# Performance work log

Hardware: AMD Instinct MI355X
Metric: run time of the kernel (lower is better)

The kernel has to match this reference:

```python
import jax, jax.numpy as jnp
import numpy as np
from jax import lax

# sym8 analysis low-pass filter (pywt.Wavelet('sym8').dec_lo, matches MATLAB Lo_D)
FL = 16
DEC_LO = np.array([-0.0033824159510061256, -0.0005421323317911481, 0.03169508781149298,
                   0.007607487324917605, -0.1432942383508097, -0.061273359067658524,
                   0.4813596512583722, 0.7771857517005235, 0.3644418948353314,
                   -0.051945838107709037, -0.027219029917056003, 0.049137179673607506,
                   0.003808752013890615, -0.01495225833704823, -0.0003029205147213668,
                   0.0018899503327594609])
REC_LO = DEC_LO[::-1]
REC_HI = ((-1.0) ** np.arange(FL)) * DEC_LO  # qmf: rec_hi[k] = (-1)^k * rec_lo[FL-1-k]
DEC_HI = REC_HI[::-1]
# lax.conv does correlation, np.convolve flips -> store flipped filters
_DEC_K = jnp.asarray(np.stack([DEC_LO[::-1], DEC_HI[::-1]])[:, None, :], dtype=jnp.float32)  # (2,1,16)
_REC_K = jnp.asarray(np.stack([REC_LO[::-1], REC_HI[::-1]])[None, :, :], dtype=jnp.float32)  # (1,2,16)
DN = ('NCH', 'OIH', 'NCH')


def _dwt(x):
    # single-level pywt dwt, mode='symmetric': pad FL-1 each side, full conv, take odd indices
    B, C, S = x.shape
    xe = jnp.pad(x.reshape(B * C, 1, S), ((0, 0), (0, 0), (FL - 1, FL - 1)), mode='symmetric')[..., 1:]
    y = lax.conv_general_dilated(xe, _DEC_K, (2,), 'VALID', dimension_numbers=DN)
    L = y.shape[-1]  # floor((S + FL - 1)/2)
    y = y.reshape(B, C, 2, L)
    return y[:, :, 0], y[:, :, 1]


def _idwt(a, d):
    # single-level pywt idwt: upsample (len 2L-1), full conv, trim FL-2 each side
    B, C, L = a.shape
    c = jnp.stack([a, d], axis=2).reshape(B * C, 2, L)
    y = lax.conv_general_dilated(c, _REC_K, (1,), [(1, 1)], lhs_dilation=(2,), dimension_numbers=DN)
    return y.reshape(B, C, y.shape[-1])  # length 2L - FL + 2


def _wavedec(x, level):
    ds = []
    a = x
    for _ in range(level):
        a, d = _dwt(a)
        ds.append(d)
    return a, ds[::-1]  # coarsest first, matching pywt [cA_n, cD_n, ..., cD_1]


def _waverec(a, ds):
    for d in ds:
        if a.shape[-1] == d.shape[-1] + 1:  # static shapes -> Python if is jit-safe
            a = a[..., :-1]
        a = _idwt(a, d)
    return a


def _c1(x, w, b):
    # 1x1 conv: w (O,C), x (B,C,L)
    return jnp.einsum('oc,bcl->bol', w, x) + b[:, None]


def _inorm(x, eps=1e-5):
    m = jnp.mean(x, axis=-1, keepdims=True)
    v = jnp.mean((x - m) ** 2, axis=-1, keepdims=True)
    return (x - m) * lax.rsqrt(v + eps)


def _block(x, w_w, w_b, ca_w, ca_b, cd_w, cd_b, m1_w, m1_b, m2_w, m2_b):
    xn = _inorm(x)
    xs = lax.conv_general_dilated(xn, w_w, (1,), [(1, 1)], dimension_numbers=DN) + w_b[:, None]
    level = cd_w.shape[0]
    a, ds = _wavedec(xn, level)
    a = _c1(a, ca_w, ca_b)
    ds = [_c1(d, cd_w[i], cd_b[i]) for i, d in enumerate(ds)]
    xw = _waverec(a, ds)[..., : xs.shape[-1]]
    xo = x + jax.nn.gelu(xw + xs, approximate=False)
    xon = _inorm(xo)
    h = jax.nn.gelu(_c1(xon, m1_w, m1_b), approximate=False)
    return xo + _c1(h, m2_w, m2_b)


def _forward(x, lift_w, lift_b, blk_w_w, blk_w_b, blk_ca_w, blk_ca_b, blk_cd_w, blk_cd_b,
             blk_m1_w, blk_m1_b, blk_m2_w, blk_m2_b, p1_w, p1_b, p2_w, p2_b):
    B, S = x.shape
    grid = jnp.broadcast_to(jnp.linspace(-1.0, 1.0, S, dtype=x.dtype)[None, None, :], (B, 1, S))
    h = jnp.concatenate([x[:, None, :], grid], axis=1)  # (B, 2, S)
    h = _c1(h, lift_w, lift_b)
    for i in range(blk_w_w.shape[0]):
        h = _block(h, blk_w_w[i], blk_w_b[i], blk_ca_w[i], blk_ca_b[i], blk_cd_w[i],
                   blk_cd_b[i], blk_m1_w[i], blk_m1_b[i], blk_m2_w[i], blk_m2_b[i])
    h = jax.nn.gelu(_c1(h, p1_w, p1_b), approximate=False)
    return _c1(h, p2_w, p2_b)


def setup_inputs():
    key = jax.random.key(0)
    ks = jax.random.split(key, 17)
    B, S, C, NB, LV = 16, 8192, 64, 4, 4
    H = 2 * C  # mlp_expansion=2
    f = jnp.float32
    rn = lambda k, shape, s: jax.random.normal(k, shape, dtype=f) * s
    return {
        'x': jax.random.normal(ks[0], (B, S), dtype=f),
        'lift_w': rn(ks[1], (C, 2), 0.5), 'lift_b': rn(ks[2], (C,), 0.05),
        'blk_w_w': rn(ks[3], (NB, C, C, 3), 0.07), 'blk_w_b': rn(ks[4], (NB, C), 0.05),
        'blk_ca_w': rn(ks[5], (NB, C, C), 0.12), 'blk_ca_b': rn(ks[6], (NB, C), 0.05),
        'blk_cd_w': rn(ks[7], (NB, LV, C, C), 0.12), 'blk_cd_b': rn(ks[8], (NB, LV, C), 0.05),
        'blk_m1_w': rn(ks[9], (NB, H, C), 0.12), 'blk_m1_b': rn(ks[10], (NB, H), 0.05),
        'blk_m2_w': rn(ks[11], (NB, C, H), 0.08), 'blk_m2_b': rn(ks[12], (NB, C), 0.05),
        'p1_w': rn(ks[13], (C // 2, C), 0.12), 'p1_b': rn(ks[14], (C // 2,), 0.05),
        'p2_w': rn(ks[15], (C, C // 2), 0.17), 'p2_b': rn(ks[16], (C,), 0.05),
    }


def reference(x, lift_w, lift_b, blk_w_w, blk_w_b, blk_ca_w, blk_ca_b, blk_cd_w, blk_cd_b,
              blk_m1_w, blk_m1_b, blk_m2_w, blk_m2_b, p1_w, p1_b, p2_w, p2_b):
    return _forward(x, lift_w, lift_b, blk_w_w, blk_w_b, blk_ca_w, blk_ca_b, blk_cd_w,
                    blk_cd_b, blk_m1_w, blk_m1_b, blk_m2_w, blk_m2_b, p1_w, p1_b, p2_w, p2_b)
```

## Files before the change

### kernel.cpp

```cpp
#include <hip/hip_runtime.h>
#include <math.h>

#define S_LEN 8192
#define B_N   16
#define NBC   1024
#define L1v 4103
#define L2v 2059
#define L3v 1037
#define L4v 526
#define LP1 4104
#define LP2 2060
#define LP3 1040
#define LP4 528

typedef __attribute__((ext_vector_type(8))) short bf16x8;
typedef __attribute__((ext_vector_type(4))) float f32x4;

__constant__ float c_dlo[16] = {
    -0.0033824159510061256f, -0.0005421323317911481f,  0.03169508781149298f,
     0.007607487324917605f,  -0.1432942383508097f,    -0.061273359067658524f,
     0.4813596512583722f,     0.7771857517005235f,     0.3644418948353314f,
    -0.05194583810770904f,   -0.027219029917056003f,   0.049137179673607506f,
     0.003808752013890615f,  -0.01495225833704823f,   -0.0003029205147213668f,
     0.0018899503327594609f
};
__constant__ float c_dhi[16] = {
    -0.0018899503327594609f, -0.0003029205147213668f,  0.01495225833704823f,
     0.003808752013890615f,  -0.049137179673607506f,  -0.027219029917056003f,
     0.05194583810770904f,    0.3644418948353314f,    -0.7771857517005235f,
     0.4813596512583722f,     0.061273359067658524f,  -0.1432942383508097f,
    -0.007607487324917605f,   0.03169508781149298f,    0.0005421323317911481f,
    -0.0033824159510061256f
};

__device__ __forceinline__ float gelu1(float x) {
    return 0.5f * x * (1.0f + erff(x * 0.70710678118654752f));
}
__device__ __forceinline__ float4 load4g(const float* __restrict__ row, int l, int L) {
    float4 v;
    if (l >= 0 && l + 3 < L) {
        v = *(const float4*)(row + l);
    } else {
        v.x = (l     >= 0 && l     < L) ? row[l]     : 0.f;
        v.y = (l + 1 >= 0 && l + 1 < L) ? row[l + 1] : 0.f;
        v.z = (l + 2 >= 0 && l + 2 < L) ? row[l + 2] : 0.f;
        v.w = (l + 3 >= 0 && l + 3 < L) ? row[l + 3] : 0.f;
    }
    return v;
}
__device__ __forceinline__ void store4g(float* __restrict__ row, int l, int L, float4 v) {
    if (l + 3 < L) {
        *(float4*)(row + l) = v;
    } else {
        if (l     < L) row[l]     = v.x;
        if (l + 1 < L) row[l + 1] = v.y;
        if (l + 2 < L) row[l + 2] = v.z;
        if (l + 3 < L) row[l + 3] = v.w;
    }
}
__device__ __forceinline__ ushort f2bf(float f) {
    uint u = __float_as_uint(f);
    u += 0x7fffu + ((u >> 16) & 1u);
    return (ushort)(u >> 16);
}
__device__ __forceinline__ uint pack2bf(float a, float b) {
    return (uint)f2bf(a) | ((uint)f2bf(b) << 16);
}

__global__ __launch_bounds__(256) void lift_kernel(const float* __restrict__ x,
                                                   const float* __restrict__ w,
                                                   const float* __restrict__ bias,
                                                   float* __restrict__ out) {
    int idx = blockIdx.x * 256 + threadIdx.x;
    int s = idx & (S_LEN - 1);
    int r = idx >> 13;
    int o = r & 63;
    int b = r >> 6;
    float g = -1.0f + 2.0f * (float)s / (float)(S_LEN - 1);
    out[idx] = fmaf(w[o * 2 + 0], x[b * S_LEN + s], fmaf(w[o * 2 + 1], g, bias[o]));
}

__global__ __launch_bounds__(256) void stats_kernel(const float* __restrict__ in,
                                                    float2* __restrict__ stats) {
    const int base = blockIdx.x * S_LEN;
    const int tid = threadIdx.x;
    float s = 0.f, ss = 0.f;
#pragma unroll
    for (int i = 0; i < 8; ++i) {
        float4 v = *(const float4*)(in + base + (tid + i * 256) * 4);
        s += v.x + v.y + v.z + v.w;
        ss = fmaf(v.x, v.x, fmaf(v.y, v.y, fmaf(v.z, v.z, fmaf(v.w, v.w, ss))));
    }
    for (int off = 32; off > 0; off >>= 1) {
        s  += __shfl_down(s, off, 64);
        ss += __shfl_down(ss, off, 64);
    }
    __shared__ float sh[8];
    int lane = tid & 63, wv = tid >> 6;
    if (lane == 0) { sh[wv] = s; sh[4 + wv] = ss; }
    __syncthreads();
    if (tid == 0) {
        float tot  = sh[0] + sh[1] + sh[2] + sh[3];
        float tot2 = sh[4] + sh[5] + sh[6] + sh[7];
        float mean = tot * (1.0f / S_LEN);
        float var  = tot2 * (1.0f / S_LEN) - mean * mean;
        stats[blockIdx.x] = make_float2(mean, rsqrtf(var + 1e-5f));
    }
}

#define CWP 200
#define CXP 72

__global__ __launch_bounds__(256) void conv3_mfma_kernel(const float* __restrict__ in,
                                                         float* __restrict__ out,
                                                         const float* __restrict__ W,
                                                         const float* __restrict__ bias,
                                                         const float2* __restrict__ stats) {
    __shared__ ushort sW[64 * CWP];
    __shared__ ushort sXt[144 * CXP];
    const int b = blockIdx.y;
    const int n0 = blockIdx.x * 128;
    const int tid = threadIdx.x;

    {
        const int o = tid >> 2, q = tid & 3;
        const float* wsrc = W + o * 192;
        uint* dst = (uint*)(sW + o * CWP + q * 48);
#pragma unroll
        for (int i = 0; i < 12; ++i) {
            int k = q * 48 + i * 4;
            int tap = k >> 6, c = k & 63;
            float v0 = wsrc[c * 3 + tap];
            float v1 = wsrc[(c + 1) * 3 + tap];
            float v2 = wsrc[(c + 2) * 3 + tap];
            float v3 = wsrc[(c + 3) * 3 + tap];
            dst[2 * i]     = pack2bf(v0, v1);
            dst[2 * i + 1] = pack2bf(v2, v3);
        }
    }
    {
        const int ch = tid >> 2, q = tid & 3;
        const int rowi = b * 64 + ch;
        const float2 st = stats[rowi];
        const float* row = in + (size_t)rowi * S_LEN;
#pragma unroll
        for (int i = 0; i < 9; ++i) {
            int p = q * 36 + i * 4;
            int l = n0 - 8 + p;
            float4 v;
            if (l >= 0 && l + 3 < S_LEN) {
                v = *(const float4*)(row + l);
                v.x = (v.x - st.x) * st.y; v.y = (v.y - st.x) * st.y;
                v.z = (v.z - st.x) * st.y; v.w = (v.w - st.x) * st.y;
            } else {
                v.x = (l     >= 0 && l     < S_LEN) ? (row[l]     - st.x) * st.y : 0.f;
                v.y = (l + 1 >= 0 && l + 1 < S_LEN) ? (row[l + 1] - st.x) * st.y : 0.f;
                v.z = (l + 2 >= 0 && l + 2 < S_LEN) ? (row[l + 2] - st.x) * st.y : 0.f;
                v.w = (l + 3 >= 0 && l + 3 < S_LEN) ? (row[l + 3] - st.x) * st.y : 0.f;
            }
            sXt[(p + 0) * CXP + ch] = f2bf(v.x);
            sXt[(p + 1) * CXP + ch] = f2bf(v.y);
            sXt[(p + 2) * CXP + ch] = f2bf(v.z);
            sXt[(p + 3) * CXP + ch] = f2bf(v.w);
        }
    }
    __syncthreads();

    const int w = tid >> 6, l = tid & 63, g = l >> 4, c = l & 15;
    f32x4 acc[2][4];
#pragma unroll
    for (int mt = 0; mt < 4; ++mt) {
        float4 bv = *(const float4*)(bias + 16 * mt + 4 * g);
#pragma unroll
        for (int t = 0; t < 2; ++t) {
            acc[t][mt][0] = bv.x; acc[t][mt][1] = bv.y;
            acc[t][mt][2] = bv.z; acc[t][mt][3] = bv.w;
        }
    }
#pragma unroll
    for (int kk = 0; kk < 6; ++kk) {
        const int tap = kk >> 1;
        bf16x8 af[4];
#pragma unroll
        for (int mt = 0; mt < 4; ++mt)
            af[mt] = *(bf16x8*)(sW + (16 * mt + c) * CWP + kk * 32 + 8 * g);
#pragma unroll
        for (int t = 0; t < 2; ++t) {
            const int nl = 32 * w + 16 * t + c;
            const int p = nl + tap + 7;
            bf16x8 xb = *(bf16x8*)(sXt + p * CXP + (kk & 1) * 32 + 8 * g);
#pragma unroll
            for (int mt = 0; mt < 4; ++mt)
                acc[t][mt] = __builtin_amdgcn_mfma_f32_16x16x32_bf16(af[mt], xb, acc[t][mt], 0, 0, 0);
        }
    }
#pragma unroll
    for (int t = 0; t < 2; ++t) {
        const int nl = 32 * w + 16 * t + c;
#pragma unroll
        for (int mt = 0; mt < 4; ++mt)
#pragma unroll
            for (int r = 0; r < 4; ++r) {
                int m = 16 * mt + 4 * g + r;
                out[((size_t)(b * 64 + m)) * S_LEN + n0 + nl] = acc[t][mt][r];
            }
    }
}

#define WMP 72
#define WXP 136

__global__ __launch_bounds__(256) void wmix_kernel(float* __restrict__ d1,
                                                   float* __restrict__ d2,
                                                   float* __restrict__ d3,
                                                   float* __restrict__ d4,
                                                   float* __restrict__ a4,
                                                   const float* __restrict__ cd_w,
                                                   const float* __restrict__ cd_b,
                                                   const float* __restrict__ ca_w,
                                                   const float* __restrict__ ca_b) {
    __shared__ ushort sW[64 * WMP];
    __shared__ ushort sX[64 * WXP];
    const int b = blockIdx.y;
    const int t = blockIdx.x;
    float* buf; const float* W; const float* bias; int L, LP, l0;
    if (t < 33)      { buf = d1; W = cd_w + 3 * 4096; bias = cd_b + 3 * 64; L = L1v; LP = LP1; l0 = t * 128; }
    else if (t < 50) { buf = d2; W = cd_w + 2 * 4096; bias = cd_b + 2 * 64; L = L2v; LP = LP2; l0 = (t - 33) * 128; }
    else if (t < 59) { buf = d3; W = cd_w + 1 * 4096; bias = cd_b + 1 * 64; L = L3v; LP = LP3; l0 = (t - 50) * 128; }
    else if (t < 64) { buf = d4; W = cd_w;            bias = cd_b;          L = L4v; LP = LP4; l0 = (t - 59) * 128; }
    else             { buf = a4; W = ca_w;            bias = ca_b;          L = L4v; LP = LP4; l0 = (t - 64) * 128; }
    const int tid = threadIdx.x;
    {
        int row = tid >> 2, q = tid & 3;
        const float* src = W + row * 64 + q * 16;
        uint* dst = (uint*)(sW + row * WMP + q * 16);
#pragma unroll
        for (int i = 0; i < 4; ++i) {
            float4 v = *(const float4*)(src + 4 * i);
            dst[2 * i]     = pack2bf(v.x, v.y);
            dst[2 * i + 1] = pack2bf(v.z, v.w);
        }
    }
    {
        int ch = tid >> 2, part = tid & 3;
        const float* src = buf + ((size_t)(b * 64 + ch)) * LP;
        uint* dst = (uint*)(sX + ch * WXP + part * 32);
#pragma unroll
        for (int i = 0; i < 8; ++i) {
            int l = l0 + part * 32 + 4 * i;
            float4 v = load4g(src, l, L);
            dst[2 * i]     = pack2bf(v.x, v.y);
            dst[2 * i + 1] = pack2bf(v.z, v.w);
        }
    }
    __syncthreads();
    const int w = tid >> 6, l = tid & 63, g = l >> 4, c = l & 15;
    f32x4 acc[2][4];
#pragma unroll
    for (int mt = 0; mt < 4; ++mt) {
        float4 bv = *(const float4*)(bias + 16 * mt + 4 * g);
#pragma unroll
        for (int tt = 0; tt < 2; ++tt) {
            acc[tt][mt][0] = bv.x; acc[tt][mt][1] = bv.y;
            acc[tt][mt][2] = bv.z; acc[tt][mt][3] = bv.w;
        }
    }
#pragma unroll
    for (int kk = 0; kk < 2; ++kk) {
        bf16x8 af[4];
#pragma unroll
        for (int mt = 0; mt < 4; ++mt)
            af[mt] = *(bf16x8*)(sW + (16 * mt + c) * WMP + kk * 32 + 8 * g);
#pragma unroll
        for (int tt = 0; tt < 2; ++tt) {
            const int nl = 32 * w + 16 * tt + c;
            bf16x8 xb;
#pragma unroll
            for (int j = 0; j < 8; ++j)
                xb[j] = (short)sX[(kk * 32 + 8 * g + j) * WXP + nl];
#pragma unroll
            for (int mt = 0; mt < 4; ++mt)
                acc[tt][mt] = __builtin_amdgcn_mfma_f32_16x16x32_bf16(af[mt], xb, acc[tt][mt], 0, 0, 0);
        }
    }
#pragma unroll
    for (int tt = 0; tt < 2; ++tt) {
        const int nl = 32 * w + 16 * tt + c;
        if (l0 + nl < L) {
#pragma unroll
            for (int mt = 0; mt < 4; ++mt)
#pragma unroll
                for (int r = 0; r < 4; ++r) {
                    int m = 16 * mt + 4 * g + r;
                    buf[((size_t)(b * 64 + m)) * LP + l0 + nl] = acc[tt][mt][r];
                }
        }
    }
}

#define W1P 72
#define W2P 136
#define XP  66
#define MP  136

__global__ __launch_bounds__(256) void mlp_kernel(float* __restrict__ A,
                                                  const float2* __restrict__ stats,
                                                  const float* __restrict__ W1,
                                                  const float* __restrict__ b1,
                                                  const float* __restrict__ W2,
                                                  const float* __restrict__ b2) {
    __shared__ ushort sW1[128 * W1P];
    __shared__ ushort sW2[64 * W2P];
    __shared__ ushort sX [64 * XP];
    __shared__ ushort sMid[64 * MP];
    const int b  = blockIdx.y;
    const int n0 = blockIdx.x * 64;
    const int tid = threadIdx.x;

    {
        int row = tid >> 1, half = tid & 1;
        const float* src = W1 + row * 64 + half * 32;
        uint* dst = (uint*)(sW1 + row * W1P + half * 32);
#pragma unroll
        for (int i = 0; i < 8; ++i) {
            float4 v = *(const float4*)(src + 4 * i);
            dst[2 * i]     = pack2bf(v.x, v.y);
            dst[2 * i + 1] = pack2bf(v.z, v.w);
        }
    }
    {
        int row = tid >> 2, q = tid & 3;
        const float* src = W2 + row * 128 + q * 32;
        uint* dst = (uint*)(sW2 + row * W2P + q * 32);
#pragma unroll
        for (int i = 0; i < 8; ++i) {
            float4 v = *(const float4*)(src + 4 * i);
            dst[2 * i]     = pack2bf(v.x, v.y);
            dst[2 * i + 1] = pack2bf(v.z, v.w);
        }
    }
    {
        int ch = tid >> 2, part = tid & 3;
        float2 st = stats[b * 64 + ch];
        const float* src = A + ((size_t)(b * 64 + ch)) * S_LEN + n0 + part * 16;
        uint* dst = (uint*)(sX + ch * XP + part * 16);
#pragma unroll
        for (int i = 0; i < 4; ++i) {
            float4 v = *(const float4*)(src + 4 * i);
            v.x = (v.x - st.x) * st.y; v.y = (v.y - st.x) * st.y;
            v.z = (v.z - st.x) * st.y; v.w = (v.w - st.x) * st.y;
            dst[2 * i]     = pack2bf(v.x, v.y);
            dst[2 * i + 1] = pack2bf(v.z, v.w);
        }
    }
    __syncthreads();

    const int w = tid >> 6;
    const int l = tid & 63;
    const int g = l >> 4;
    const int c = l & 15;
    const int nl = 16 * w + c;

    bf16x8 xb[2];
#pragma unroll
    for (int kk = 0; kk < 2; ++kk)
#pragma unroll
        for (int j = 0; j < 8; ++j)
            xb[kk][j] = (short)sX[(kk * 32 + 8 * g + j) * XP + nl];

    f32x4 acc1[8];
#pragma unroll
    for (int mt = 0; mt < 8; ++mt) {
        float4 bv = *(const float4*)(b1 + 16 * mt + 4 * g);
        acc1[mt][0] = bv.x; acc1[mt][1] = bv.y; acc1[mt][2] = bv.z; acc1[mt][3] = bv.w;
    }
#pragma unroll
    for (int kk = 0; kk < 2; ++kk) {
#pragma unroll
        for (int mt = 0; mt < 8; ++mt) {
            bf16x8 af = *(bf16x8*)(sW1 + (16 * mt + c) * W1P + kk * 32 + 8 * g);
            acc1[mt] = __builtin_amdgcn_mfma_f32_16x16x32_bf16(af, xb[kk], acc1[mt], 0, 0, 0);
        }
    }
#pragma unroll
    for (int mt = 0; mt < 8; ++mt)
#pragma unroll
        for (int r = 0; r < 4; ++r)
            sMid[nl * MP + 16 * mt + 4 * g + r] = f2bf(gelu1(acc1[mt][r]));

    bf16x8 mb[4];
#pragma unroll
    for (int kk = 0; kk < 4; ++kk)
        mb[kk] = *(bf16x8*)(sMid + nl * MP + kk * 32 + 8 * g);

    f32x4 acc2[4];
#pragma unroll
    for (int mt = 0; mt < 4; ++mt) {
        float4 bv = *(const float4*)(b2 + 16 * mt + 4 * g);
        acc2[mt][0] = bv.x; acc2[mt][1] = bv.y; acc2[mt][2] = bv.z; acc2[mt][3] = bv.w;
    }
#pragma unroll
    for (int kk = 0; kk < 4; ++kk) {
#pragma unroll
        for (int mt = 0; mt < 4; ++mt) {
            bf16x8 af = *(bf16x8*)(sW2 + (16 * mt + c) * W2P + kk * 32 + 8 * g);
            acc2[mt] = __builtin_amdgcn_mfma_f32_16x16x32_bf16(af, mb[kk], acc2[mt], 0, 0, 0);
        }
    }
#pragma unroll
    for (int mt = 0; mt < 4; ++mt) {
#pragma unroll
        for (int r = 0; r < 4; ++r) {
            int m = 16 * mt + 4 * g + r;
            float* p = A + ((size_t)(b * 64 + m)) * S_LEN + n0 + nl;
            *p = acc2[mt][r] + *p;
        }
    }
}

#define HXP 66
#define HMP 40

__global__ __launch_bounds__(256) void head_kernel(const float* __restrict__ A,
                                                   float* __restrict__ out,
                                                   const float* __restrict__ W1,
                                                   const float* __restrict__ b1,
                                                   const float* __restrict__ W2,
                                                   const float* __restrict__ b2) {
    __shared__ ushort sW1[32 * 72];
    __shared__ ushort sW2[64 * HMP];
    __shared__ ushort sX [64 * HXP];
    __shared__ ushort sMid[64 * HMP];
    const int b = blockIdx.y, n0 = blockIdx.x * 64, tid = threadIdx.x;
    {
        int row = tid >> 3, q = tid & 7;
        const float* src = W1 + row * 64 + q * 8;
        uint* dst = (uint*)(sW1 + row * 72 + q * 8);
#pragma unroll
        for (int i = 0; i < 2; ++i) {
            float4 v = *(const float4*)(src + 4 * i);
            dst[2 * i] = pack2bf(v.x, v.y); dst[2 * i + 1] = pack2bf(v.z, v.w);
        }
    }
    {
        int row = tid >> 2, q = tid & 3;
        const float* src = W2 + row * 32 + q * 8;
        uint* dst = (uint*)(sW2 + row * HMP + q * 8);
#pragma unroll
        for (int i = 0; i < 2; ++i) {
            float4 v = *(const float4*)(src + 4 * i);
            dst[2 * i] = pack2bf(v.x, v.y); dst[2 * i + 1] = pack2bf(v.z, v.w);
        }
    }
    {
        int ch = tid >> 2, part = tid & 3;
        const float* src = A + ((size_t)(b * 64 + ch)) * S_LEN + n0 + part * 16;
        uint* dst = (uint*)(sX + ch * HXP + part * 16);
#pragma unroll
        for (int i = 0; i < 4; ++i) {
            float4 v = *(const float4*)(src + 4 * i);
            dst[2 * i] = pack2bf(v.x, v.y); dst[2 * i + 1] = pack2bf(v.z, v.w);
        }
    }
    __syncthreads();
    const int w = tid >> 6, l = tid & 63, g = l >> 4, c = l & 15;
    const int nl = 16 * w + c;
    bf16x8 xb[2];
#pragma unroll
    for (int kk = 0; kk < 2; ++kk)
#pragma unroll
        for (int j = 0; j < 8; ++j)
            xb[kk][j] = (short)sX[(kk * 32 + 8 * g + j) * HXP + nl];
    f32x4 acc1[2];
#pragma unroll
    for (int mt = 0; mt < 2; ++mt) {
        float4 bv = *(const float4*)(b1 + 16 * mt + 4 * g);
        acc1[mt][0] = bv.x; acc1[mt][1] = bv.y; acc1[mt][2] = bv.z; acc1[mt][3] = bv.w;
    }
#pragma unroll
    for (int kk = 0; kk < 2; ++kk)
#pragma unroll
        for (int mt = 0; mt < 2; ++mt) {
            bf16x8 af = *(bf16x8*)(sW1 + (16 * mt + c) * 72 + kk * 32 + 8 * g);
            acc1[mt] = __builtin_amdgcn_mfma_f32_16x16x32_bf16(af, xb[kk], acc1[mt], 0, 0, 0);
        }
#pragma unroll
    for (int mt = 0; mt < 2; ++mt)
#pragma unroll
        for (int r = 0; r < 4; ++r)
            sMid[nl * HMP + 16 * mt + 4 * g + r] = f2bf(gelu1(acc1[mt][r]));
    bf16x8 mb = *(bf16x8*)(sMid + nl * HMP + 8 * g);
    f32x4 acc2[4];
#pragma unroll
    for (int mt = 0; mt < 4; ++mt) {
        float4 bv = *(const float4*)(b2 + 16 * mt + 4 * g);
        acc2[mt][0] = bv.x; acc2[mt][1] = bv.y; acc2[mt][2] = bv.z; acc2[mt][3] = bv.w;
    }
#pragma unroll
    for (int mt = 0; mt < 4; ++mt) {
        bf16x8 af = *(bf16x8*)(sW2 + (16 * mt + c) * HMP + 8 * g);
        acc2[mt] = __builtin_amdgcn_mfma_f32_16x16x32_bf16(af, mb, acc2[mt], 0, 0, 0);
    }
#pragma unroll
    for (int mt = 0; mt < 4; ++mt)
#pragma unroll
        for (int r = 0; r < 4; ++r) {
            int m = 16 * mt + 4 * g + r;
            out[((size_t)(b * 64 + m)) * S_LEN + n0 + nl] = acc2[mt][r];
        }
}

__device__ __forceinline__ void dwt8_core(const float* __restrict__ xb,
                                          float* __restrict__ lo, float* __restrict__ hi) {
#pragma unroll
    for (int j = 0; j < 8; ++j) {
        float l0 = 0.f, h0 = 0.f;
#pragma unroll
        for (int k = 0; k < 16; ++k) {
            float v = xb[2 * j + k + 2];
            l0 = fmaf(v, c_dlo[15 - k], l0);
            h0 = fmaf(v, c_dhi[15 - k], h0);
        }
        lo[j] = l0; hi[j] = h0;
    }
}

__device__ __forceinline__ void dwt_lds_v2(const float* __restrict__ in, int Sin,
                                           float* __restrict__ aout,
                                           float* __restrict__ dout_g, int Lout, int tid) {
    const int NT = (Lout + 7) >> 3;
    for (int g = tid; g < NT; g += 256) {
        float xb[32];
        const int base = 16 * g - 16;
        if (base >= 0 && base + 32 <= Sin) {
#pragma unroll
            for (int q = 0; q < 8; ++q)
                *(float4*)(xb + 4 * q) = *(const float4*)(in + base + 4 * q);
        } else {
#pragma unroll
            for (int loc = 0; loc < 32; ++loc) {
                int i = base + loc;
                i = (i < 0) ? (-1 - i) : i;
                i = (i >= Sin) ? (2 * Sin - 1 - i) : i;
                xb[loc] = in[i];
            }
        }
        float lo[8], hi[8];
        dwt8_core(xb, lo, hi);
        const int t0 = 8 * g;
        if (t0 + 8 <= Lout) {
            *(float4*)(aout + t0)     = make_float4(lo[0], lo[1], lo[2], lo[3]);
            *(float4*)(aout + t0 + 4) = make_float4(lo[4], lo[5], lo[6], lo[7]);
        } else {
#pragma unroll
            for (int j = 0; j < 8; ++j) if (t0 + j < Lout) aout[t0 + j] = lo[j];
        }
        store4g(dout_g, t0,     Lout, make_float4(hi[0], hi[1], hi[2], hi[3]));
        store4g(dout_g, t0 + 4, Lout, make_float4(hi[4], hi[5], hi[6], hi[7]));
    }
}

__global__ __launch_bounds__(256) void dwt_full_kernel(const float* __restrict__ A,
                                                       const float2* __restrict__ stats,
                                                       float* __restrict__ d1,
                                                       float* __restrict__ d2,
                                                       float* __restrict__ d3,
                                                       float* __restrict__ d4,
                                                       float* __restrict__ a4) {
    __shared__ float bufA[4104];
    __shared__ float bufB[2060];
    const int row = blockIdx.x;
    const int tid = threadIdx.x;
    const float2 st = stats[row];
    const float* x = A + (size_t)row * S_LEN;
    float* d1r = d1 + (size_t)row * LP1;

    for (int g = tid; g < 513; g += 256) {
        const int base = 16 * g - 16;
        float xb[32];
        if (base >= 0 && base + 32 <= S_LEN) {
#pragma unroll
            for (int q = 0; q < 8; ++q) {
                float4 v = *(const float4*)(x + base + 4 * q);
                v.x = (v.x - st.x) * st.y; v.y = (v.y - st.x) * st.y;
                v.z = (v.z - st.x) * st.y; v.w = (v.w - st.x) * st.y;
                *(float4*)(xb + 4 * q) = v;
            }
        } else {
#pragma unroll
            for (int loc = 0; loc < 32; ++loc) {
                int i = base + loc;
                i = (i < 0) ? (-1 - i) : i;
                i = (i >= S_LEN) ? (2 * S_LEN - 1 - i) : i;
                xb[loc] = (x[i] - st.x) * st.y;
            }
        }
        float lo[8], hi[8];
        dwt8_core(xb, lo, hi);
        const int t0 = 8 * g;
#pragma unroll
        for (int j = 0; j < 8; ++j)
            if (t0 + j < L1v) bufA[t0 + j] = lo[j];
        store4g(d1r, t0,     L1v, make_float4(hi[0], hi[1], hi[2], hi[3]));
        store4g(d1r, t0 + 4, L1v, make_float4(hi[4], hi[5], hi[6], hi[7]));
    }
    __syncthreads();
    dwt_lds_v2(bufA, L1v, bufB, d2 + (size_t)row * LP2, L2v, tid);
    __syncthreads();
    dwt_lds_v2(bufB, L2v, bufA, d3 + (size_t)row * LP3, L3v, tid);
    __syncthreads();
    dwt_lds_v2(bufA, L3v, bufB, d4 + (size_t)row * LP4, L4v, tid);
    __syncthreads();
    float* a4r = a4 + (size_t)row * LP4;
    for (int i = tid; i < 132; i += 256)
        *(float4*)(a4r + 4 * i) = *(const float4*)(bufB + 4 * i);
}

__device__ __forceinline__ void idwt8_regs(const float* __restrict__ a,
                                           const float* __restrict__ d,
                                           int g, int Lc, float* __restrict__ y) {
    float av[12], dv[12];
    const int m0 = 4 * g;
    if (m0 + 12 <= Lc) {
#pragma unroll
        for (int q = 0; q < 3; ++q) {
            *(float4*)(av + 4 * q) = *(const float4*)(a + m0 + 4 * q);
            *(float4*)(dv + 4 * q) = *(const float4*)(d + m0 + 4 * q);
        }
    } else {
#pragma unroll
        for (int jj = 0; jj < 12; ++jj) {
            int m = m0 + jj;
            bool ok = (m < Lc);
            av[jj] = ok ? a[m] : 0.f;
            dv[jj] = ok ? d[m] : 0.f;
        }
    }
#pragma unroll
    for (int e = 0; e < 4; ++e) {
        float ye = 0.f, yo = 0.f;
#pragma unroll
        for (int j = 0; j < 8; ++j) {
            ye = fmaf(av[e + j], c_dlo[2 * j + 1], ye);
            ye = fmaf(dv[e + j], c_dlo[14 - 2 * j], ye);
            yo = fmaf(av[e + j], c_dlo[2 * j], yo);
            yo = fmaf(dv[e + j], -c_dlo[15 - 2 * j], yo);
        }
        y[2 * e] = ye;
        y[2 * e + 1] = yo;
    }
}

__device__ __forceinline__ void idwt_lds_v2(const float* __restrict__ a,
                                            const float* __restrict__ d,
                                            int Lc, int Lout, float* __restrict__ out, int tid) {
    const int NT = (Lout + 7) >> 3;
    for (int g = tid; g < NT; g += 256) {
        float y[8];
        idwt8_regs(a, d, g, Lc, y);
        const int t0 = 8 * g;
        if (t0 + 8 <= Lout) {
            *(float4*)(out + t0)     = make_float4(y[0], y[1], y[2], y[3]);
            *(float4*)(out + t0 + 4) = make_float4(y[4], y[5], y[6], y[7]);
        } else {
#pragma unroll
            for (int j = 0; j < 8; ++j) if (t0 + j < Lout) out[t0 + j] = y[j];
        }
    }
}

__device__ __forceinline__ void gload_lds(const float* __restrict__ src, int Lv,
                                          float* __restrict__ dst, int tid) {
    const int NG = (Lv + 3) >> 2;
    for (int i = tid; i < NG; i += 256)
        *(float4*)(dst + 4 * i) = load4g(src, 4 * i, Lv);
}

__global__ __launch_bounds__(256) void idwt_full_kernel(const float* __restrict__ a4,
                                                        const float* __restrict__ d4,
                                                        const float* __restrict__ d3,
                                                        const float* __restrict__ d2,
                                                        const float* __restrict__ d1,
                                                        float* __restrict__ h,
                                                        const float* __restrict__ xs,
                                                        float2* __restrict__ statsOut) {
    __shared__ float bufY[4104];
    __shared__ float bufA[4104];
    __shared__ float bufD[4104];
    const int row = blockIdx.x;
    const int tid = threadIdx.x;

    gload_lds(a4 + (size_t)row * LP4, L4v, bufA, tid);
    gload_lds(d4 + (size_t)row * LP4, L4v, bufD, tid);
    __syncthreads();
    idwt_lds_v2(bufA, bufD, L4v, 1038, bufY, tid);
    __syncthreads();
    gload_lds(d3 + (size_t)row * LP3, L3v, bufD, tid);
    __syncthreads();
    idwt_lds_v2(bufY, bufD, L3v, 2060, bufA, tid);
    __syncthreads();
    gload_lds(d2 + (size_t)row * LP2, L2v, bufD, tid);
    __syncthreads();
    idwt_lds_v2(bufA, bufD, L2v, 4104, bufY, tid);
    __syncthreads();
    gload_lds(d1 + (size_t)row * LP1, L1v, bufD, tid);
    __syncthreads();

    float* hrow = h + (size_t)row * S_LEN;
    const float* srow = xs + (size_t)row * S_LEN;
    float s = 0.f, ss = 0.f;
#pragma unroll
    for (int it = 0; it < 4; ++it) {
        const int g = it * 256 + tid;
        float y[8];
        idwt8_regs(bufY, bufD, g, L1v, y);
        const int t0 = 8 * g;
#pragma unroll
        for (int q = 0; q < 2; ++q) {
            float4 sv = *(const float4*)(srow + t0 + 4 * q);
            float4 hv = *(const float4*)(hrow + t0 + 4 * q);
            hv.x += gelu1(y[4 * q + 0] + sv.x);
            hv.y += gelu1(y[4 * q + 1] + sv.y);
            hv.z += gelu1(y[4 * q + 2] + sv.z);
            hv.w += gelu1(y[4 * q + 3] + sv.w);
            *(float4*)(hrow + t0 + 4 * q) = hv;
            s += hv.x + hv.y + hv.z + hv.w;
            ss = fmaf(hv.x, hv.x, fmaf(hv.y, hv.y, fmaf(hv.z, hv.z, fmaf(hv.w, hv.w, ss))));
        }
    }
    for (int off = 32; off > 0; off >>= 1) {
        s  += __shfl_down(s, off, 64);
        ss += __shfl_down(ss, off, 64);
    }
    __syncthreads();
    int lane = tid & 63, wv = tid >> 6;
    if (lane == 0) { bufA[wv] = s; bufA[4 + wv] = ss; }
    __syncthreads();
    if (tid == 0) {
        float tot  = bufA[0] + bufA[1] + bufA[2] + bufA[3];
        float tot2 = bufA[4] + bufA[5] + bufA[6] + bufA[7];
        float mean = tot * (1.0f / S_LEN);
        float var  = tot2 * (1.0f / S_LEN) - mean * mean;
        statsOut[row] = make_float2(mean, rsqrtf(var + 1e-5f));
    }
}

extern "C" void kernel_launch(void* const* d_in, const int* in_sizes, int n_in,
                              void* d_out, int out_size, void* d_ws, size_t ws_size,
                              hipStream_t stream) {
    const float* x       = (const float*)d_in[0];
    const float* lift_w  = (const float*)d_in[1];
    const float* lift_b  = (const float*)d_in[2];
    const float* blk_w_w = (const float*)d_in[3];
    const float* blk_w_b = (const float*)d_in[4];
    const float* blk_ca_w= (const float*)d_in[5];
    const float* blk_ca_b= (const float*)d_in[6];
    const float* blk_cd_w= (const float*)d_in[7];
    const float* blk_cd_b= (const float*)d_in[8];
    const float* blk_m1_w= (const float*)d_in[9];
    const float* blk_m1_b= (const float*)d_in[10];
    const float* blk_m2_w= (const float*)d_in[11];
    const float* blk_m2_b= (const float*)d_in[12];
    const float* p1_w    = (const float*)d_in[13];
    const float* p1_b    = (const float*)d_in[14];
    const float* p2_w    = (const float*)d_in[15];
    const float* p2_b    = (const float*)d_in[16];

    float* ws = (float*)d_ws;
    const size_t T32 = (size_t)NBC * S_LEN;
    float* A  = ws;
    float* Cc = ws + 2 * T32;
    float* d1 = ws + 4 * T32;
    float* d2 = d1 + (size_t)NBC * LP1;
    float* d3 = d2 + (size_t)NBC * LP2;
    float* d4 = d3 + (size_t)NBC * LP3;
    float* ap0 = d4 + (size_t)NBC * LP4;
    float* ap1 = ap0 + (size_t)NBC * 4104;
    float2* statsBuf = (float2*)(ap1 + (size_t)NBC * 4104);

    dim3 blk(256);

    lift_kernel<<<(NBC * S_LEN) / 256, blk, 0, stream>>>(x, lift_w, lift_b, A);

    for (int i = 0; i < 4; ++i) {
        const float* w_w  = blk_w_w  + (size_t)i * 64 * 64 * 3;
        const float* w_b  = blk_w_b  + (size_t)i * 64;
        const float* ca_w = blk_ca_w + (size_t)i * 64 * 64;
        const float* ca_b = blk_ca_b + (size_t)i * 64;
        const float* cd_w = blk_cd_w + (size_t)i * 4 * 64 * 64;
        const float* cd_b = blk_cd_b + (size_t)i * 4 * 64;
        const float* m1_w = blk_m1_w + (size_t)i * 128 * 64;
        const float* m1_b = blk_m1_b + (size_t)i * 128;
        const float* m2_w = blk_m2_w + (size_t)i * 64 * 128;
        const float* m2_b = blk_m2_b + (size_t)i * 64;

        stats_kernel<<<NBC, blk, 0, stream>>>(A, statsBuf);
        conv3_mfma_kernel<<<dim3(S_LEN / 128, B_N), blk, 0, stream>>>(A, Cc, w_w, w_b, statsBuf);
        dwt_full_kernel<<<NBC, blk, 0, stream>>>(A, statsBuf, d1, d2, d3, d4, ap1);

        wmix_kernel<<<dim3(69, B_N), blk, 0, stream>>>(d1, d2, d3, d4, ap1,
                                                       cd_w, cd_b, ca_w, ca_b);

        idwt_full_kernel<<<NBC, blk, 0, stream>>>(ap1, d4, d3, d2, d1, A, Cc, statsBuf);
        mlp_kernel<<<dim3(S_LEN / 64, B_N), blk, 0, stream>>>(A, statsBuf, m1_w, m1_b, m2_w, m2_b);
    }

    head_kernel<<<dim3(S_LEN / 64, B_N), blk, 0, stream>>>(A, (float*)d_out,
                                                           p1_w, p1_b, p2_w, p2_b);
}
```

Baseline: 828.7 us.

## Pre-convert all weights to bf16 once and enlarge MLP tiles

A new prep kernel converts every layer's weights to bf16 in a packed workspace buffer, with the conv weights pre-permuted into tap-major order. Each later kernel then copies ready bf16 rows into shared memory with vector loads instead of converting fp32 weights in every block. The MLP kernel also changes: it reads weights straight from global/L2 rather than staging them in LDS, and each block covers 128 positions instead of 64. That halves the grid and frees LDS, but it adds an extra launch and depends on L2 hits for the weight fragment loads.

```diff
diff --git a/kernel.cpp b/kernel.cpp
--- a/kernel.cpp
+++ b/kernel.cpp
@@ -12,6 +12,15 @@
 #define LP2 2060
 #define LP3 1040
 #define LP4 528
+
+#define OFF_CONV 0
+#define OFF_M1   49152
+#define OFF_M2   81920
+#define OFF_CD   114688
+#define OFF_CA   180224
+#define OFF_P1   196608
+#define OFF_P2   198656
+#define WTOT     200704
 
 typedef __attribute__((ext_vector_type(8))) short bf16x8;
 typedef __attribute__((ext_vector_type(4))) float f32x4;
@@ -67,6 +76,31 @@
     return (uint)f2bf(a) | ((uint)f2bf(b) << 16);
 }
 
+__global__ __launch_bounds__(256) void prep_kernel(const float* __restrict__ convW,
+                                                   const float* __restrict__ m1,
+                                                   const float* __restrict__ m2,
+                                                   const float* __restrict__ cd,
+                                                   const float* __restrict__ ca,
+                                                   const float* __restrict__ p1,
+                                                   const float* __restrict__ p2,
+                                                   ushort* __restrict__ wbuf) {
+    int idx = blockIdx.x * 256 + threadIdx.x;
+    if (idx >= WTOT) return;
+    float v;
+    if (idx < OFF_M1) {
+        int i = idx / 12288, r = idx % 12288;
+        int o = r / 192, k = r % 192;
+        int tap = k >> 6, c = k & 63;
+        v = convW[i * 12288 + o * 192 + c * 3 + tap];
+    } else if (idx < OFF_M2) v = m1[idx - OFF_M1];
+    else if (idx < OFF_CD)   v = m2[idx - OFF_M2];
+    else if (idx < OFF_CA)   v = cd[idx - OFF_CD];
+    else if (idx < OFF_P1)   v = ca[idx - OFF_CA];
+    else if (idx < OFF_P2)   v = p1[idx - OFF_P1];
+    else                     v = p2[idx - OFF_P2];
+    wbuf[idx] = f2bf(v);
+}
+
 __global__ __launch_bounds__(256) void lift_kernel(const float* __restrict__ x,
                                                    const float* __restrict__ w,
                                                    const float* __restrict__ bias,
@@ -113,7 +147,7 @@
 
 __global__ __launch_bounds__(256) void conv3_mfma_kernel(const float* __restrict__ in,
                                                          float* __restrict__ out,
-                                                         const float* __restrict__ W,
+                                                         const ushort* __restrict__ Wbf,
                                                          const float* __restrict__ bias,
                                                          const float2* __restrict__ stats) {
     __shared__ ushort sW[64 * CWP];
@@ -124,19 +158,10 @@
 
     {
         const int o = tid >> 2, q = tid & 3;
-        const float* wsrc = W + o * 192;
-        uint* dst = (uint*)(sW + o * CWP + q * 48);
-#pragma unroll
-        for (int i = 0; i < 12; ++i) {
-            int k = q * 48 + i * 4;
-            int tap = k >> 6, c = k & 63;
-            float v0 = wsrc[c * 3 + tap];
-            float v1 = wsrc[(c + 1) * 3 + tap];
-            float v2 = wsrc[(c + 2) * 3 + tap];
-            float v3 = wsrc[(c + 3) * 3 + tap];
-            dst[2 * i]     = pack2bf(v0, v1);
-            dst[2 * i + 1] = pack2bf(v2, v3);
-        }
+        const uint4* src = (const uint4*)(Wbf + o * 192 + q * 48);
+        uint4* dst = (uint4*)(sW + o * CWP + q * 48);
+#pragma unroll
+        for (int i = 0; i < 6; ++i) dst[i] = src[i];
     }
     {
         const int ch = tid >> 2, q = tid & 3;
@@ -215,31 +240,26 @@
                                                    float* __restrict__ d3,
                                                    float* __restrict__ d4,
                                                    float* __restrict__ a4,
-                                                   const float* __restrict__ cd_w,
+                                                   const ushort* __restrict__ cdbf,
                                                    const float* __restrict__ cd_b,
-                                                   const float* __restrict__ ca_w,
+                                                   const ushort* __restrict__ cabf,
                                                    const float* __restrict__ ca_b) {
     __shared__ ushort sW[64 * WMP];
     __shared__ ushort sX[64 * WXP];
     const int b = blockIdx.y;
     const int t = blockIdx.x;
-    float* buf; const float* W; const float* bias; int L, LP, l0;
-    if (t < 33)      { buf = d1; W = cd_w + 3 * 4096; bias = cd_b + 3 * 64; L = L1v; LP = LP1; l0 = t * 128; }
-    else if (t < 50) { buf = d2; W = cd_w + 2 * 4096; bias = cd_b + 2 * 64; L = L2v; LP = LP2; l0 = (t - 33) * 128; }
-    else if (t < 59) { buf = d3; W = cd_w + 1 * 4096; bias = cd_b + 1 * 64; L = L3v; LP = LP3; l0 = (t - 50) * 128; }
-    else if (t < 64) { buf = d4; W = cd_w;            bias = cd_b;          L = L4v; LP = LP4; l0 = (t - 59) * 128; }
-    else             { buf = a4; W = ca_w;            bias = ca_b;          L = L4v; LP = LP4; l0 = (t - 64) * 128; }
+    float* buf; const ushort* W; const float* bias; int L, LP, l0;
+    if (t < 33)      { buf = d1; W = cdbf + 3 * 4096; bias = cd_b + 3 * 64; L = L1v; LP = LP1; l0 = t * 128; }
+    else if (t < 50) { buf = d2; W = cdbf + 2 * 4096; bias = cd_b + 2 * 64; L = L2v; LP = LP2; l0 = (t - 33) * 128; }
+    else if (t < 59) { buf = d3; W = cdbf + 1 * 4096; bias = cd_b + 1 * 64; L = L3v; LP = LP3; l0 = (t - 50) * 128; }
+    else if (t < 64) { buf = d4; W = cdbf;            bias = cd_b;          L = L4v; LP = LP4; l0 = (t - 59) * 128; }
+    else             { buf = a4; W = cabf;            bias = ca_b;          L = L4v; LP = LP4; l0 = (t - 64) * 128; }
     const int tid = threadIdx.x;
     {
         int row = tid >> 2, q = tid & 3;
-        const float* src = W + row * 64 + q * 16;
-        uint* dst = (uint*)(sW + row * WMP + q * 16);
-#pragma unroll
-        for (int i = 0; i < 4; ++i) {
-            float4 v = *(const float4*)(src + 4 * i);
-            dst[2 * i]     = pack2bf(v.x, v.y);
-            dst[2 * i + 1] = pack2bf(v.z, v.w);
-        }
+        const uint4* src = (const uint4*)(W + row * 64 + q * 16);
+        uint4* dst = (uint4*)(sW + row * WMP + q * 16);
+        dst[0] = src[0]; dst[1] = src[1];
     }
     {
         int ch = tid >> 2, part = tid & 3;
@@ -298,54 +318,28 @@
     }
 }
 
-#define W1P 72
-#define W2P 136
-#define XP  66
-#define MP  136
+#define XP2 132
+#define MP2 136
 
 __global__ __launch_bounds__(256) void mlp_kernel(float* __restrict__ A,
                                                   const float2* __restrict__ stats,
-                                                  const float* __restrict__ W1,
+                                                  const ushort* __restrict__ W1bf,
                                                   const float* __restrict__ b1,
-                                                  const float* __restrict__ W2,
+                                                  const ushort* __restrict__ W2bf,
                                                   const float* __restrict__ b2) {
-    __shared__ ushort sW1[128 * W1P];
-    __shared__ ushort sW2[64 * W2P];
-    __shared__ ushort sX [64 * XP];
-    __shared__ ushort sMid[64 * MP];
+    __shared__ ushort sX [64 * XP2];
+    __shared__ ushort sMid[128 * MP2];
     const int b  = blockIdx.y;
-    const int n0 = blockIdx.x * 64;
+    const int n0 = blockIdx.x * 128;
     const int tid = threadIdx.x;
 
-    {
-        int row = tid >> 1, half = tid & 1;
-        const float* src = W1 + row * 64 + half * 32;
-        uint* dst = (uint*)(sW1 + row * W1P + half * 32);
-#pragma unroll
-        for (int i = 0; i < 8; ++i) {
-            float4 v = *(const float4*)(src + 4 * i);
-            dst[2 * i]     = pack2bf(v.x, v.y);
-            dst[2 * i + 1] = pack2bf(v.z, v.w);
-        }
-    }
-    {
-        int row = tid >> 2, q = tid & 3;
-        const float* src = W2 + row * 128 + q * 32;
-        uint* dst = (uint*)(sW2 + row * W2P + q * 32);
-#pragma unroll
-        for (int i = 0; i < 8; ++i) {
-            float4 v = *(const float4*)(src + 4 * i);
-            dst[2 * i]     = pack2bf(v.x, v.y);
-            dst[2 * i + 1] = pack2bf(v.z, v.w);
-        }
-    }
     {
         int ch = tid >> 2, part = tid & 3;
         float2 st = stats[b * 64 + ch];
-        const float* src = A + ((size_t)(b * 64 + ch)) * S_LEN + n0 + part * 16;
-        uint* dst = (uint*)(sX + ch * XP + part * 16);
-#pragma unroll
-        for (int i = 0; i < 4; ++i) {
+        const float* src = A + ((size_t)(b * 64 + ch)) * S_LEN + n0 + part * 32;
+        uint* dst = (uint*)(sX + ch * XP2 + part * 32);
+#pragma unroll
+        for (int i = 0; i < 8; ++i) {
             float4 v = *(const float4*)(src + 4 * i);
             v.x = (v.x - st.x) * st.y; v.y = (v.y - st.x) * st.y;
             v.z = (v.z - st.x) * st.y; v.w = (v.w - st.x) * st.y;
@@ -355,66 +349,66 @@
     }
     __syncthreads();
 
-    const int w = tid >> 6;
-    const int l = tid & 63;
-    const int g = l >> 4;
-    const int c = l & 15;
-    const int nl = 16 * w + c;
-
-    bf16x8 xb[2];
-#pragma unroll
-    for (int kk = 0; kk < 2; ++kk)
-#pragma unroll
-        for (int j = 0; j < 8; ++j)
-            xb[kk][j] = (short)sX[(kk * 32 + 8 * g + j) * XP + nl];
-
-    f32x4 acc1[8];
-#pragma unroll
-    for (int mt = 0; mt < 8; ++mt) {
-        float4 bv = *(const float4*)(b1 + 16 * mt + 4 * g);
-        acc1[mt][0] = bv.x; acc1[mt][1] = bv.y; acc1[mt][2] = bv.z; acc1[mt][3] = bv.w;
-    }
-#pragma unroll
-    for (int kk = 0; kk < 2; ++kk) {
+    const int w = tid >> 6, l = tid & 63, g = l >> 4, c = l & 15;
+
+#pragma unroll
+    for (int tt = 0; tt < 2; ++tt) {
+        const int nl = 32 * w + 16 * tt + c;
+        bf16x8 xb[2];
+#pragma unroll
+        for (int kk = 0; kk < 2; ++kk)
+#pragma unroll
+            for (int j = 0; j < 8; ++j)
+                xb[kk][j] = (short)sX[(kk * 32 + 8 * g + j) * XP2 + nl];
+        f32x4 acc1[8];
 #pragma unroll
         for (int mt = 0; mt < 8; ++mt) {
-            bf16x8 af = *(bf16x8*)(sW1 + (16 * mt + c) * W1P + kk * 32 + 8 * g);
-            acc1[mt] = __builtin_amdgcn_mfma_f32_16x16x32_bf16(af, xb[kk], acc1[mt], 0, 0, 0);
-        }
-    }
-#pragma unroll
-    for (int mt = 0; mt < 8; ++mt)
-#pragma unroll
-        for (int r = 0; r < 4; ++r)
-            sMid[nl * MP + 16 * mt + 4 * g + r] = f2bf(gelu1(acc1[mt][r]));
-
-    bf16x8 mb[4];
-#pragma unroll
-    for (int kk = 0; kk < 4; ++kk)
-        mb[kk] = *(bf16x8*)(sMid + nl * MP + kk * 32 + 8 * g);
-
-    f32x4 acc2[4];
-#pragma unroll
-    for (int mt = 0; mt < 4; ++mt) {
-        float4 bv = *(const float4*)(b2 + 16 * mt + 4 * g);
-        acc2[mt][0] = bv.x; acc2[mt][1] = bv.y; acc2[mt][2] = bv.z; acc2[mt][3] = bv.w;
-    }
-#pragma unroll
-    for (int kk = 0; kk < 4; ++kk) {
+            float4 bv = *(const float4*)(b1 + 16 * mt + 4 * g);
+            acc1[mt][0] = bv.x; acc1[mt][1] = bv.y; acc1[mt][2] = bv.z; acc1[mt][3] = bv.w;
+        }
+#pragma unroll
+        for (int kk = 0; kk < 2; ++kk)
+#pragma unroll
+            for (int mt = 0; mt < 8; ++mt) {
+                bf16x8 af = *(const bf16x8*)(W1bf + (16 * mt + c) * 64 + kk * 32 + 8 * g);
+                acc1[mt] = __builtin_amdgcn_mfma_f32_16x16x32_bf16(af, xb[kk], acc1[mt], 0, 0, 0);
+            }
+#pragma unroll
+        for (int mt = 0; mt < 8; ++mt) {
+            uint* mp = (uint*)(sMid + nl * MP2 + 16 * mt + 4 * g);
+            mp[0] = pack2bf(gelu1(acc1[mt][0]), gelu1(acc1[mt][1]));
+            mp[1] = pack2bf(gelu1(acc1[mt][2]), gelu1(acc1[mt][3]));
+        }
+    }
+
+#pragma unroll
+    for (int tt = 0; tt < 2; ++tt) {
+        const int nl = 32 * w + 16 * tt + c;
+        bf16x8 mb[4];
+#pragma unroll
+        for (int kk = 0; kk < 4; ++kk)
+            mb[kk] = *(bf16x8*)(sMid + nl * MP2 + kk * 32 + 8 * g);
+        f32x4 acc2[4];
 #pragma unroll
         for (int mt = 0; mt < 4; ++mt) {
-            bf16x8 af = *(bf16x8*)(sW2 + (16 * mt + c) * W2P + kk * 32 + 8 * g);
-            acc2[mt] = __builtin_amdgcn_mfma_f32_16x16x32_bf16(af, mb[kk], acc2[mt], 0, 0, 0);
-        }
-    }
-#pragma unroll
-    for (int mt = 0; mt < 4; ++mt) {
-#pragma unroll
-        for (int r = 0; r < 4; ++r) {
-            int m = 16 * mt + 4 * g + r;
-            float* p = A + ((size_t)(b * 64 + m)) * S_LEN + n0 + nl;
-            *p = acc2[mt][r] + *p;
-        }
+            float4 bv = *(const float4*)(b2 + 16 * mt + 4 * g);
+            acc2[mt][0] = bv.x; acc2[mt][1] = bv.y; acc2[mt][2] = bv.z; acc2[mt][3] = bv.w;
+        }
+#pragma unroll
+        for (int kk = 0; kk < 4; ++kk)
+#pragma unroll
+            for (int mt = 0; mt < 4; ++mt) {
+                bf16x8 af = *(const bf16x8*)(W2bf + (16 * mt + c) * 128 + kk * 32 + 8 * g);
+                acc2[mt] = __builtin_amdgcn_mfma_f32_16x16x32_bf16(af, mb[kk], acc2[mt], 0, 0, 0);
+            }
+#pragma unroll
+        for (int mt = 0; mt < 4; ++mt)
+#pragma unroll
+            for (int r = 0; r < 4; ++r) {
+                int m = 16 * mt + 4 * g + r;
+                float* p = A + ((size_t)(b * 64 + m)) * S_LEN + n0 + nl;
+                *p = acc2[mt][r] + *p;
+            }
     }
 }
 
@@ -423,9 +417,9 @@
 
 __global__ __launch_bounds__(256) void head_kernel(const float* __restrict__ A,
                                                    float* __restrict__ out,
-                                                   const float* __restrict__ W1,
+                                                   const ushort* __restrict__ W1bf,
                                                    const float* __restrict__ b1,
-                                                   const float* __restrict__ W2,
+                                                   const ushort* __restrict__ W2bf,
                                                    const float* __restrict__ b2) {
     __shared__ ushort sW1[32 * 72];
     __shared__ ushort sW2[64 * HMP];
@@ -434,23 +428,11 @@
     const int b = blockIdx.y, n0 = blockIdx.x * 64, tid = threadIdx.x;
     {
         int row = tid >> 3, q = tid & 7;
-        const float* src = W1 + row * 64 + q * 8;
-        uint* dst = (uint*)(sW1 + row * 72 + q * 8);
-#pragma unroll
-        for (int i = 0; i < 2; ++i) {
-            float4 v = *(const float4*)(src + 4 * i);
-            dst[2 * i] = pack2bf(v.x, v.y); dst[2 * i + 1] = pack2bf(v.z, v.w);
-        }
+        *(uint4*)(sW1 + row * 72 + q * 8) = *(const uint4*)(W1bf + row * 64 + q * 8);
     }
     {
         int row = tid >> 2, q = tid & 3;
-        const float* src = W2 + row * 32 + q * 8;
-        uint* dst = (uint*)(sW2 + row * HMP + q * 8);
-#pragma unroll
-        for (int i = 0; i < 2; ++i) {
-            float4 v = *(const float4*)(src + 4 * i);
-            dst[2 * i] = pack2bf(v.x, v.y); dst[2 * i + 1] = pack2bf(v.z, v.w);
-        }
+        *(uint4*)(sW2 + row * HMP + q * 8) = *(const uint4*)(W2bf + row * 32 + q * 8);
     }
     {
         int ch = tid >> 2, part = tid & 3;
@@ -777,34 +759,38 @@
     float* ap0 = d4 + (size_t)NBC * LP4;
     float* ap1 = ap0 + (size_t)NBC * 4104;
     float2* statsBuf = (float2*)(ap1 + (size_t)NBC * 4104);
+    ushort* wbuf = (ushort*)(statsBuf + NBC);
 
     dim3 blk(256);
 
+    prep_kernel<<<(WTOT + 255) / 256, blk, 0, stream>>>(blk_w_w, blk_m1_w, blk_m2_w,
+                                                        blk_cd_w, blk_ca_w, p1_w, p2_w, wbuf);
     lift_kernel<<<(NBC * S_LEN) / 256, blk, 0, stream>>>(x, lift_w, lift_b, A);
 
     for (int i = 0; i < 4; ++i) {
-        const float* w_w  = blk_w_w  + (size_t)i * 64 * 64 * 3;
         const float* w_b  = blk_w_b  + (size_t)i * 64;
-        const float* ca_w = blk_ca_w + (size_t)i * 64 * 64;
         const float* ca_b = blk_ca_b + (size_t)i * 64;
-        const float* cd_w = blk_cd_w + (size_t)i * 4 * 64 * 64;
         const float* cd_b = blk_cd_b + (size_t)i * 4 * 64;
-        const float* m1_w = blk_m1_w + (size_t)i * 128 * 64;
         const float* m1_b = blk_m1_b + (size_t)i * 128;
-        const float* m2_w = blk_m2_w + (size_t)i * 64 * 128;
         const float* m2_b = blk_m2_b + (size_t)i * 64;
+        const ushort* convbf = wbuf + OFF_CONV + (size_t)i * 12288;
+        const ushort* m1bf   = wbuf + OFF_M1   + (size_t)i * 8192;
+        const ushort* m2bf   = wbuf + OFF_M2   + (size_t)i * 8192;
+        const ushort* cdbf   = wbuf + OFF_CD   + (size_t)i * 16384;
+        const ushort* cabf   = wbuf + OFF_CA   + (size_t)i * 4096;
 
         stats_kernel<<<NBC, blk, 0, stream>>>(A, statsBuf);
-        conv3_mfma_kernel<<<dim3(S_LEN / 128, B_N), blk, 0, stream>>>(A, Cc, w_w, w_b, statsBuf);
+        conv3_mfma_kernel<<<dim3(S_LEN / 128, B_N), blk, 0, stream>>>(A, Cc, convbf, w_b, statsBuf);
         dwt_full_kernel<<<NBC, blk, 0, stream>>>(A, statsBuf, d1, d2, d3, d4, ap1);
 
         wmix_kernel<<<dim3(69, B_N), blk, 0, stream>>>(d1, d2, d3, d4, ap1,
-                                                       cd_w, cd_b, ca_w, ca_b);
+                                                       cdbf, cd_b, cabf, ca_b);
 
         idwt_full_kernel<<<NBC, blk, 0, stream>>>(ap1, d4, d3, d2, d1, A, Cc, statsBuf);
-        mlp_kernel<<<dim3(S_LEN / 64, B_N), blk, 0, stream>>>(A, statsBuf, m1_w, m1_b, m2_w, m2_b);
+        mlp_kernel<<<dim3(S_LEN / 128, B_N), blk, 0, stream>>>(A, statsBuf, m1bf, m1_b, m2bf, m2_b);
     }
 
     head_kernel<<<dim3(S_LEN / 64, B_N), blk, 0, stream>>>(A, (float*)d_out,
-                                                           p1_w, p1_b, p2_w, p2_b);
-}
+                                                           wbuf + OFF_P1, p1_b,
+                                                           wbuf + OFF_P2, p2_b);
+}
```

After: 839.3 us. Within noise of the previous version (+1.3%).
